# Kernel optimization log

Measured on AMD Instinct MI355X. Metric: run time of the kernel, lower is better.

## Reference

```python
import jax, jax.numpy as jnp
import numpy as np

P_EPS = 1e-6            # nn.PairwiseDistance default eps
ALPHA = 0.25
STD_TARGET = 1.0
NUM_COMMUNITIES = 512   # C = number of unique community ids
BIG = 1e30              # masking value for hard-negative min


def setup_inputs() -> dict:
    key = jax.random.key(0)
    k1, k2, k3 = jax.random.split(key, 3)
    B, N, D, C = 1, 100000, 128, NUM_COMMUNITIES
    node_features = jax.random.normal(k1, (B, N, D), dtype=jnp.float32)
    # row 0: a permutation of node indices; row 1: community of that node.
    perm = jax.random.permutation(k2, N).astype(jnp.int32)
    comm_per_node = jnp.concatenate([
        jnp.arange(C, dtype=jnp.int32),  # guarantee every community appears
        jax.random.randint(k3, (N - C,), 0, C, dtype=jnp.int32),
    ])
    community_belong_list = jnp.stack([perm, comm_per_node[perm]])  # [2, N]
    return {"node_features": node_features, "community_belong_list": community_belong_list}


def reference(node_features, community_belong_list):
    B, N, D = node_features.shape
    C = NUM_COMMUNITIES
    dt = node_features.dtype

    # ---- _community_inverse_permute: invert row-0 permutation, reorder columns ----
    perm = community_belong_list[0]
    inv = jnp.zeros((N,), perm.dtype).at[perm].add(jnp.arange(N, dtype=perm.dtype))
    cbl = community_belong_list[:, inv]          # row0 == arange(N) after this
    comm = cbl[1]                                # [N] community id per node
    src = node_features[:, cbl[0], :]            # [B,N,D] gather (identity order)

    # ---- groupby sum / count -> community means ----
    comm_sum = jnp.zeros((B, C, D), dt).at[:, comm, :].add(src)        # [B,C,D]
    counts = jnp.zeros((C,), dt).at[comm].add(jnp.asarray(1.0, dt))   # [C]
    comm_mean = comm_sum / counts[None, :, None]                      # [B,C,D]

    # ---- cdist(node_features, comm_mean, p=2) -> [B,N,C] ----
    x2 = jnp.sum(node_features * node_features, -1)                   # [B,N]
    c2 = jnp.sum(comm_mean * comm_mean, -1)                           # [B,C]
    dots = jnp.einsum('bnd,bcd->bnc', node_features, comm_mean)
    distance = jnp.sqrt(jnp.maximum(x2[:, :, None] + c2[:, None, :] - 2.0 * dots, 0.0))

    # ---- leave-one-out community mean per node, positive distance ----
    cnt_pn = counts[comm]                                             # [N]
    cnt_m1 = jnp.maximum(cnt_pn - 1.0, 1.0)                           # [N]
    x_minus = jnp.where((cnt_pn == 1.0)[None, :, None], jnp.asarray(0.0, dt), src)
    loo_mean = (comm_sum[:, comm, :] - x_minus) / cnt_m1[None, :, None]
    pos_dist = jnp.sqrt(jnp.sum((loo_mean - src + P_EPS) ** 2, -1))   # [B,N]

    # ---- negatives: all communities except the node's own ----
    own = distance[:, jnp.arange(N), comm]                            # [B,N]
    mean_neg = (jnp.sum(distance, -1) - own) / (C - 1)                # [B,N]
    pos_mask = jnp.zeros((N, C), bool).at[jnp.arange(N), comm].set(True)
    hard_neg = jnp.min(jnp.where(pos_mask[None], jnp.asarray(BIG, dt), distance), -1)

    trip_mean = jnp.maximum(pos_dist - mean_neg + ALPHA, 0.0)
    trip_min = jnp.maximum(pos_dist - hard_neg + ALPHA, 0.0)

    # ---- groupby std (unbiased) per community per feature ----
    sq = jnp.zeros((B, C, D), dt).at[:, comm, :].add((src - comm_mean[:, comm, :]) ** 2)
    std = jnp.sqrt(sq / jnp.maximum(counts - 1.0, 1.0)[None, :, None])

    return (trip_mean.mean(), trip_min.mean(), ((std - STD_TARGET) ** 2).mean())
```

## Files before the change

### kernel.cpp

```cpp
#include <hip/hip_runtime.h>

#define NCOMM 512
#define DIM   128
#define ALPHA 0.25f
#define PEPS  1e-6f
#define BIGF  1e30f
#define TILE_C 16
#define NT    (NCOMM / TILE_C)

typedef __attribute__((ext_vector_type(8))) _Float16 f16x8;
typedef __attribute__((ext_vector_type(4))) float f32x4;

#define GLOAD_LDS16(g, l) __builtin_amdgcn_global_load_lds( \
    (const __attribute__((address_space(1))) void*)(g), \
    (__attribute__((address_space(3))) void*)(l), 16, 0, 0)


__global__ void k_prep(const int* __restrict__ cbl, int* __restrict__ comm,
                       int* __restrict__ counts, int N) {
    __shared__ int h[NCOMM];
    int t = threadIdx.x;
    h[t] = 0; h[t + 256] = 0;
    __syncthreads();
    int i = blockIdx.x * 256 + t;
    if (i < N) {
        int p = cbl[i];
        int c = cbl[N + i];
        comm[p] = c;
        atomicAdd(&h[c], 1);
    }
    __syncthreads();
    int v = h[t];        if (v) atomicAdd(&counts[t], v);
    v = h[t + 256];      if (v) atomicAdd(&counts[t + 256], v);
}

__global__ void k_scan(const int* __restrict__ counts, int* __restrict__ offsets,
                       int* __restrict__ cursor, float* __restrict__ countf) {
    __shared__ int sc[NCOMM];
    int t = threadIdx.x;
    int v0 = counts[t];
    sc[t] = v0;
    __syncthreads();
    for (int off = 1; off < NCOMM; off <<= 1) {
        int v = (t >= off) ? sc[t - off] : 0;
        __syncthreads();
        sc[t] += v;
        __syncthreads();
    }
    int excl = sc[t] - v0;
    offsets[t] = excl;
    cursor[t]  = excl;
    countf[t]  = (float)v0;
}

__global__ void k_sort(const int* __restrict__ comm, int* __restrict__ cursor,
                       int* __restrict__ sorted, int N) {
    __shared__ int h[NCOMM], hb[NCOMM];
    int t = threadIdx.x;
    h[t] = 0; h[t + 256] = 0;
    __syncthreads();
    int j0 = blockIdx.x * 1024 + t;
    int cs[4];
    #pragma unroll
    for (int q = 0; q < 4; ++q) {
        int j = j0 + q * 256;
        cs[q] = (j < N) ? comm[j] : -1;
        if (cs[q] >= 0) atomicAdd(&h[cs[q]], 1);
    }
    __syncthreads();
    int v = h[t];        if (v) hb[t] = atomicAdd(&cursor[t], v);
    v = h[t + 256];      if (v) hb[t + 256] = atomicAdd(&cursor[t + 256], v);
    __syncthreads();
    #pragma unroll
    for (int q = 0; q < 4; ++q) {
        int j = j0 + q * 256;
        if (cs[q] >= 0) {
            int p = atomicAdd(&hb[cs[q]], 1);
            sorted[p] = j;
        }
    }
}


__global__ void __launch_bounds__(256) k_stats(
        const float* __restrict__ NF,
        const int* __restrict__ sorted, const int* __restrict__ offsets,
        const int* __restrict__ counts,
        float* __restrict__ comm_sum,
        _Float16* __restrict__ CMh,
        float* __restrict__ c2, float* __restrict__ accum) {
    __shared__ int ridx[512];
    __shared__ float4 bufS[256], bufQ[256];
    int c = blockIdx.x, t = threadIdx.x;
    int d4 = t & 31, r = t >> 5;
    int cnt = counts[c], base = offsets[c];
    const float4* NF4 = (const float4*)NF;

    float4 s4 = make_float4(0.f, 0.f, 0.f, 0.f);
    float4 q4 = make_float4(0.f, 0.f, 0.f, 0.f);
    for (int chunk = 0; chunk < cnt; chunk += 512) {
        int m = min(cnt - chunk, 512);
        for (int i = t; i < m; i += 256) ridx[i] = sorted[base + chunk + i];
        __syncthreads();
        int i = r;
        for (; i + 24 < m; i += 32) {
            int a0 = ridx[i], a1 = ridx[i + 8], a2 = ridx[i + 16], a3 = ridx[i + 24];
            float4 v0 = NF4[(size_t)a0 * 32 + d4];
            float4 v1 = NF4[(size_t)a1 * 32 + d4];
            float4 v2 = NF4[(size_t)a2 * 32 + d4];
            float4 v3 = NF4[(size_t)a3 * 32 + d4];
            s4.x += v0.x; s4.y += v0.y; s4.z += v0.z; s4.w += v0.w;
            q4.x = fmaf(v0.x, v0.x, q4.x); q4.y = fmaf(v0.y, v0.y, q4.y);
            q4.z = fmaf(v0.z, v0.z, q4.z); q4.w = fmaf(v0.w, v0.w, q4.w);
            s4.x += v1.x; s4.y += v1.y; s4.z += v1.z; s4.w += v1.w;
            q4.x = fmaf(v1.x, v1.x, q4.x); q4.y = fmaf(v1.y, v1.y, q4.y);
            q4.z = fmaf(v1.z, v1.z, q4.z); q4.w = fmaf(v1.w, v1.w, q4.w);
            s4.x += v2.x; s4.y += v2.y; s4.z += v2.z; s4.w += v2.w;
            q4.x = fmaf(v2.x, v2.x, q4.x); q4.y = fmaf(v2.y, v2.y, q4.y);
            q4.z = fmaf(v2.z, v2.z, q4.z); q4.w = fmaf(v2.w, v2.w, q4.w);
            s4.x += v3.x; s4.y += v3.y; s4.z += v3.z; s4.w += v3.w;
            q4.x = fmaf(v3.x, v3.x, q4.x); q4.y = fmaf(v3.y, v3.y, q4.y);
            q4.z = fmaf(v3.z, v3.z, q4.z); q4.w = fmaf(v3.w, v3.w, q4.w);
        }
        for (; i < m; i += 8) {
            float4 v = NF4[(size_t)ridx[i] * 32 + d4];
            s4.x += v.x; s4.y += v.y; s4.z += v.z; s4.w += v.w;
            q4.x = fmaf(v.x, v.x, q4.x); q4.y = fmaf(v.y, v.y, q4.y);
            q4.z = fmaf(v.z, v.z, q4.z); q4.w = fmaf(v.w, v.w, q4.w);
        }
        __syncthreads();
    }
    bufS[t] = s4; bufQ[t] = q4;
    __syncthreads();
    if (t < 128) {
        float4 a = bufS[t], b = bufS[t + 128];
        a.x += b.x; a.y += b.y; a.z += b.z; a.w += b.w; bufS[t] = a;
        float4 e = bufQ[t], f = bufQ[t + 128];
        e.x += f.x; e.y += f.y; e.z += f.z; e.w += f.w; bufQ[t] = e;
    }
    __syncthreads();
    if (t < 64) {
        float4 a = bufS[t], b = bufS[t + 64];
        a.x += b.x; a.y += b.y; a.z += b.z; a.w += b.w; bufS[t] = a;
        float4 e = bufQ[t], f = bufQ[t + 64];
        e.x += f.x; e.y += f.y; e.z += f.z; e.w += f.w; bufQ[t] = e;
    }
    __syncthreads();
    if (t < 32) {
        float4 a = bufS[t], b = bufS[t + 32];
        a.x += b.x; a.y += b.y; a.z += b.z; a.w += b.w;
        float4 e = bufQ[t], f = bufQ[t + 32];
        e.x += f.x; e.y += f.y; e.z += f.z; e.w += f.w;
        float sarr[4] = {a.x, a.y, a.z, a.w};
        float qarr[4] = {e.x, e.y, e.z, e.w};
        float cf = (float)cnt;
        float mm = 0.f, ee = 0.f;
        #pragma unroll
        for (int k = 0; k < 4; ++k) {
            int d = t * 4 + k;
            float s = sarr[k];
            comm_sum[c * DIM + d] = s;
            float m = (cnt > 0) ? s / cf : 0.f;
            CMh[c * DIM + d] = (_Float16)m;
            float varn = fmaxf(fmaf(-cf * m, m, qarr[k]), 0.f);
            float stdv = sqrtf(varn / fmaxf(cf - 1.f, 1.f));
            float er = stdv - 1.f;
            mm = fmaf(m, m, mm);
            ee = fmaf(er, er, ee);
        }
        #pragma unroll
        for (int msk = 1; msk < 32; msk <<= 1) {
            mm += __shfl_xor(mm, msk);
            ee += __shfl_xor(ee, msk);
        }
        if (t == 0) {
            c2[c] = mm;
            atomicAdd(&accum[2], ee);
        }
    }
}


__global__ void __launch_bounds__(256, 4) k_main(
        const float* __restrict__ NF,
        const _Float16* __restrict__ CMh,
        const float* __restrict__ comm_sum,
        const float* __restrict__ c2g,
        const float* __restrict__ countf,
        const int* __restrict__ comm,
        float* __restrict__ accum, int N) {
    __shared__ _Float16 Bst[4][4][TILE_C * 64];
    __shared__ float c2s[NCOMM];
    __shared__ int   comms[128];
    __shared__ float x2sh[128];
    __shared__ float sums[128], mins[128];
    __shared__ float red[8];

    int tid = threadIdx.x;
    int w  = tid >> 6;
    int l  = tid & 63;
    int lr = l & 15;
    int lk = l >> 4;
    int n0 = blockIdx.x * 128;

    int off0 = ((l >> 3) << 7) + (((l & 7) ^ ((l >> 3) & 7)) << 3);
    const _Float16* gsrc = CMh + off0;
    auto stage = [&](int ss, int b) {
        const _Float16* g = gsrc + (size_t)(ss >> 1) * 2048 + (ss & 1) * 64;
        _Float16* lh = &Bst[w][b][0];
        GLOAD_LDS16(g,        lh);
        GLOAD_LDS16(g + 1024, lh + 512);
    };
    stage(0, 0); stage(1, 1); stage(2, 2);

    c2s[tid]       = c2g[tid];
    c2s[tid + 256] = c2g[tid + 256];
    if (tid < 128) {
        int gn = n0 + tid;
        comms[tid] = (gn < N) ? comm[gn] : -1;
    }

    f16x8 ah[2][4];
    #pragma unroll
    for (int mf = 0; mf < 2; ++mf) {
        int n = n0 + w * 32 + mf * 16 + lr;
        const float4* src = (const float4*)NF + (size_t)n * 32 + lk * 2;
        float p2 = 0.f;
        #pragma unroll
        for (int ks = 0; ks < 4; ++ks) {
            float4 v0 = make_float4(0.f, 0.f, 0.f, 0.f), v1 = v0;
            if (n < N) { v0 = src[ks * 8]; v1 = src[ks * 8 + 1]; }
            float fr[8] = {v0.x, v0.y, v0.z, v0.w, v1.x, v1.y, v1.z, v1.w};
            f16x8 hh;
            #pragma unroll
            for (int t = 0; t < 8; ++t) {
                hh[t] = (_Float16)fr[t];
                p2 = fmaf(fr[t], fr[t], p2);
            }
            ah[mf][ks] = hh;
        }
        p2 += __shfl_xor(p2, 16);
        p2 += __shfl_xor(p2, 32);
        if (lk == 0) x2sh[w * 32 + mf * 16 + lr] = -0.5f * p2;
    }
    __syncthreads();

    f32x4 x2v[2];
    int cnv[2][4];
    float sumv[2][4], minv[2][4];
    #pragma unroll
    for (int mf = 0; mf < 2; ++mf) {
        x2v[mf] = *(const f32x4*)&x2sh[w * 32 + mf * 16 + lk * 4];
        #pragma unroll
        for (int j = 0; j < 4; ++j) {
            cnv[mf][j] = comms[w * 32 + mf * 16 + lk * 4 + j];
            sumv[mf][j] = 0.f; minv[mf][j] = BIGF;
        }
    }

    for (int tt = 0; tt < NT; ++tt) {
        f32x4 acc0, acc1;
        {
            int ssn = 2 * tt + 3;
            if (ssn < 64) stage(ssn, ssn & 3);
            if (tt <= 30) { asm volatile("s_waitcnt vmcnt(6)" ::: "memory"); }
            else          { asm volatile("s_waitcnt vmcnt(2)" ::: "memory"); }
            __builtin_amdgcn_sched_barrier(0);
            const _Float16* bp = &Bst[w][(2 * tt) & 3][0];
            acc0 = x2v[0]; acc1 = x2v[1];
            #pragma unroll
            for (int ks2 = 0; ks2 < 2; ++ks2) {
                int ch = (ks2 * 4 + lk) ^ (lr & 7);
                f16x8 b = *(const f16x8*)&bp[(size_t)(lr * 64 + ch * 8)];
                acc0 = __builtin_amdgcn_mfma_f32_16x16x32_f16(ah[0][ks2], b, acc0, 0, 0, 0);
                acc1 = __builtin_amdgcn_mfma_f32_16x16x32_f16(ah[1][ks2], b, acc1, 0, 0, 0);
            }
        }
        {
            int ssn = 2 * tt + 4;
            if (ssn < 64) stage(ssn, ssn & 3);
            if (tt <= 29)      { asm volatile("s_waitcnt vmcnt(6)" ::: "memory"); }
            else if (tt == 30) { asm volatile("s_waitcnt vmcnt(4)" ::: "memory"); }
            else               { asm volatile("s_waitcnt vmcnt(0)" ::: "memory"); }
            __builtin_amdgcn_sched_barrier(0);
            const _Float16* bp = &Bst[w][(2 * tt + 1) & 3][0];
            #pragma unroll
            for (int ks2 = 0; ks2 < 2; ++ks2) {
                int ch = (ks2 * 4 + lk) ^ (lr & 7);
                f16x8 b = *(const f16x8*)&bp[(size_t)(lr * 64 + ch * 8)];
                acc0 = __builtin_amdgcn_mfma_f32_16x16x32_f16(ah[0][2 + ks2], b, acc0, 0, 0, 0);
                acc1 = __builtin_amdgcn_mfma_f32_16x16x32_f16(ah[1][2 + ks2], b, acc1, 0, 0, 0);
            }
            int ccol = tt * TILE_C + lr;
            float c2v = c2s[ccol];
            #pragma unroll
            for (int j = 0; j < 4; ++j) {
                float d2a = fmaf(-2.f, acc0[j], c2v);
                float da  = __builtin_amdgcn_sqrtf(fmaxf(d2a, 0.f));
                sumv[0][j] += da;
                minv[0][j] = fminf(minv[0][j], (cnv[0][j] == ccol) ? BIGF : da);
                float d2b = fmaf(-2.f, acc1[j], c2v);
                float db  = __builtin_amdgcn_sqrtf(fmaxf(d2b, 0.f));
                sumv[1][j] += db;
                minv[1][j] = fminf(minv[1][j], (cnv[1][j] == ccol) ? BIGF : db);
            }
        }
    }

    #pragma unroll
    for (int mf = 0; mf < 2; ++mf)
        #pragma unroll
        for (int j = 0; j < 4; ++j) {
            float sv = sumv[mf][j], mv = minv[mf][j];
            #pragma unroll
            for (int msk = 1; msk < 16; msk <<= 1) {
                sv += __shfl_xor(sv, msk);
                mv = fminf(mv, __shfl_xor(mv, msk));
            }
            if (lr == 0) {
                int idx = w * 32 + mf * 16 + lk * 4 + j;
                sums[idx] = sv; mins[idx] = mv;
            }
        }
    __syncthreads();

    float tmean = 0.f, tminv = 0.f;
    {
        int ln = tid >> 1, half = tid & 1;
        int n = n0 + ln;
        if (n < N) {
            int cnode = comms[ln];
            float cf  = countf[cnode];
            float cm1 = fmaxf(cf - 1.f, 1.f);
            float rs  = 1.f / cm1;
            bool single = (cf == 1.f);
            const float4* srow = (const float4*)NF + (size_t)n * 32 + half * 16;
            const float4* csum = (const float4*)(comm_sum + (size_t)cnode * DIM) + half * 16;
            float q = 0.f, dot = 0.f;
            #pragma unroll
            for (int m = 0; m < 16; ++m) {
                float4 sv = srow[m];
                float4 cs = csum[m];
                float4 xm = single ? make_float4(0.f, 0.f, 0.f, 0.f) : sv;
                float lx = (cs.x - xm.x) * rs - sv.x + PEPS;
                float ly = (cs.y - xm.y) * rs - sv.y + PEPS;
                float lz = (cs.z - xm.z) * rs - sv.z + PEPS;
                float lw = (cs.w - xm.w) * rs - sv.w + PEPS;
                q = fmaf(lx, lx, fmaf(ly, ly, fmaf(lz, lz, fmaf(lw, lw, q))));
                dot = fmaf(sv.x, cs.x, fmaf(sv.y, cs.y, fmaf(sv.z, cs.z, fmaf(sv.w, cs.w, dot))));
            }
            q   += __shfl_xor(q, 1);
            dot += __shfl_xor(dot, 1);
            if (half == 0) {
                float pos = sqrtf(q);
                float x2 = -2.f * x2sh[ln];
                float ownd2 = x2 + c2s[cnode] - 2.f * (dot / cf);
                float own = sqrtf(fmaxf(ownd2, 0.f));
                float mean_neg = (sums[ln] - own) * (1.f / (float)(NCOMM - 1));
                tmean = fmaxf(pos - mean_neg + ALPHA, 0.f);
                tminv = fmaxf(pos - mins[ln] + ALPHA, 0.f);
            }
        }
    }
    #pragma unroll
    for (int msk = 1; msk < 64; msk <<= 1) {
        tmean += __shfl_xor(tmean, msk);
        tminv += __shfl_xor(tminv, msk);
    }
    if ((tid & 63) == 0) { red[w * 2] = tmean; red[w * 2 + 1] = tminv; }
    __syncthreads();
    if (tid == 0) {
        atomicAdd(&accum[0], red[0] + red[2] + red[4] + red[6]);
        atomicAdd(&accum[1], red[1] + red[3] + red[5] + red[7]);
    }
}

__global__ void k_final(const float* __restrict__ accum, float* __restrict__ out, int N) {
    if (threadIdx.x == 0) {
        out[0] = accum[0] / (float)N;
        out[1] = accum[1] / (float)N;
        out[2] = accum[2] / (float)(NCOMM * DIM);
    }
}


extern "C" void kernel_launch(void* const* d_in, const int* in_sizes, int n_in,
                              void* d_out, int out_size, void* d_ws, size_t ws_size,
                              hipStream_t stream) {
    const float* NF  = (const float*)d_in[0];
    const int*   CBL = (const int*)d_in[1];
    int N = in_sizes[1] / 2;
    if (N <= 0) return;

    char* ws = (char*)d_ws;
    float* accum   = (float*)ws;
    int*   counts  = (int*)(ws + 16);
    int*   cursor  = (int*)(ws + 16 + 2048);
    int*   offsets = (int*)(ws + 16 + 2 * 2048);
    float* countf  = (float*)(ws + 16 + 3 * 2048);
    float* c2      = (float*)(ws + 16 + 4 * 2048);
    char* p = ws + 16 + 5 * 2048;
    int* comm   = (int*)p; p += (size_t)N * 4;
    int* sorted = (int*)p; p += (size_t)N * 4;
    float* comm_sum = (float*)p; p += (size_t)NCOMM * DIM * 4;
    _Float16* CMh = (_Float16*)p;

    hipMemsetAsync(d_ws, 0, 16 + 2048, stream);

    int nb = (N + 255) / 256;
    k_prep<<<nb, 256, 0, stream>>>(CBL, comm, counts, N);
    k_scan<<<1, NCOMM, 0, stream>>>(counts, offsets, cursor, countf);
    int nb4 = (N + 1023) / 1024;
    k_sort<<<nb4, 256, 0, stream>>>(comm, cursor, sorted, N);
    k_stats<<<NCOMM, 256, 0, stream>>>(NF, sorted, offsets, counts,
                                       comm_sum, CMh, c2, accum);
    int mb = (N + 127) / 128;
    k_main<<<mb, 256, 0, stream>>>(NF, CMh, comm_sum, c2, countf,
                                   comm, accum, N);
    k_final<<<1, 64, 0, stream>>>(accum, (float*)d_out, N);
}
```

Before: 119.6 us.

## Fold scan and final kernels into last-block epilogues, unroll stats gather, raise MFMA priority

Removes the separate k_scan and k_final launches. The last block to finish k_prep now does the 512-entry prefix scan, and the last block of k_main writes the outputs, both detected with an atomic done counter. The gather loop in k_stats is unrolled from 4 to 8 loads per iteration to keep more memory requests in flight, and s_setprio wraps the MFMA sections in k_main. The aim is less launch overhead and better latency hiding, at the cost of extra atomics, threadfences and more register pressure.

```diff
diff --git a/kernel.cpp b/kernel.cpp
--- a/kernel.cpp
+++ b/kernel.cpp
@@ -17,8 +17,12 @@
 
 
 __global__ void k_prep(const int* __restrict__ cbl, int* __restrict__ comm,
-                       int* __restrict__ counts, int N) {
+                       int* __restrict__ counts, int* __restrict__ done,
+                       int* __restrict__ cursor, int* __restrict__ offsets,
+                       float* __restrict__ countf, int N) {
     __shared__ int h[NCOMM];
+    __shared__ int sc[NCOMM];
+    __shared__ int lastFlag;
     int t = threadIdx.x;
     h[t] = 0; h[t + 256] = 0;
     __syncthreads();
@@ -32,25 +36,30 @@
     __syncthreads();
     int v = h[t];        if (v) atomicAdd(&counts[t], v);
     v = h[t + 256];      if (v) atomicAdd(&counts[t + 256], v);
-}
-
-__global__ void k_scan(const int* __restrict__ counts, int* __restrict__ offsets,
-                       int* __restrict__ cursor, float* __restrict__ countf) {
-    __shared__ int sc[NCOMM];
-    int t = threadIdx.x;
-    int v0 = counts[t];
-    sc[t] = v0;
+
+    __threadfence();
+    __syncthreads();
+    if (t == 0) lastFlag = (atomicAdd(done, 1) == (int)gridDim.x - 1) ? 1 : 0;
+    __syncthreads();
+    if (!lastFlag) return;
+
+    int a0 = atomicAdd(&counts[t], 0);
+    int a1 = atomicAdd(&counts[t + 256], 0);
+    sc[t] = a0; sc[t + 256] = a1;
     __syncthreads();
     for (int off = 1; off < NCOMM; off <<= 1) {
-        int v = (t >= off) ? sc[t - off] : 0;
+        int x0 = (t >= off) ? sc[t - off] : 0;
+        int x1 = (t + 256 >= off) ? sc[t + 256 - off] : 0;
         __syncthreads();
-        sc[t] += v;
+        sc[t] += x0; sc[t + 256] += x1;
         __syncthreads();
     }
-    int excl = sc[t] - v0;
-    offsets[t] = excl;
-    cursor[t]  = excl;
-    countf[t]  = (float)v0;
+    offsets[t]       = sc[t] - a0;
+    cursor[t]        = sc[t] - a0;
+    countf[t]        = (float)a0;
+    offsets[t + 256] = sc[t + 256] - a1;
+    cursor[t + 256]  = sc[t + 256] - a1;
+    countf[t + 256]  = (float)a1;
 }
 
 __global__ void k_sort(const int* __restrict__ comm, int* __restrict__ cursor,
@@ -103,12 +112,17 @@
         for (int i = t; i < m; i += 256) ridx[i] = sorted[base + chunk + i];
         __syncthreads();
         int i = r;
-        for (; i + 24 < m; i += 32) {
-            int a0 = ridx[i], a1 = ridx[i + 8], a2 = ridx[i + 16], a3 = ridx[i + 24];
+        for (; i + 56 < m; i += 64) {
+            int a0 = ridx[i],      a1 = ridx[i + 8],  a2 = ridx[i + 16], a3 = ridx[i + 24];
+            int a4 = ridx[i + 32], a5 = ridx[i + 40], a6 = ridx[i + 48], a7 = ridx[i + 56];
             float4 v0 = NF4[(size_t)a0 * 32 + d4];
             float4 v1 = NF4[(size_t)a1 * 32 + d4];
             float4 v2 = NF4[(size_t)a2 * 32 + d4];
             float4 v3 = NF4[(size_t)a3 * 32 + d4];
+            float4 v4 = NF4[(size_t)a4 * 32 + d4];
+            float4 v5 = NF4[(size_t)a5 * 32 + d4];
+            float4 v6 = NF4[(size_t)a6 * 32 + d4];
+            float4 v7 = NF4[(size_t)a7 * 32 + d4];
             s4.x += v0.x; s4.y += v0.y; s4.z += v0.z; s4.w += v0.w;
             q4.x = fmaf(v0.x, v0.x, q4.x); q4.y = fmaf(v0.y, v0.y, q4.y);
             q4.z = fmaf(v0.z, v0.z, q4.z); q4.w = fmaf(v0.w, v0.w, q4.w);
@@ -121,6 +135,18 @@
             s4.x += v3.x; s4.y += v3.y; s4.z += v3.z; s4.w += v3.w;
             q4.x = fmaf(v3.x, v3.x, q4.x); q4.y = fmaf(v3.y, v3.y, q4.y);
             q4.z = fmaf(v3.z, v3.z, q4.z); q4.w = fmaf(v3.w, v3.w, q4.w);
+            s4.x += v4.x; s4.y += v4.y; s4.z += v4.z; s4.w += v4.w;
+            q4.x = fmaf(v4.x, v4.x, q4.x); q4.y = fmaf(v4.y, v4.y, q4.y);
+            q4.z = fmaf(v4.z, v4.z, q4.z); q4.w = fmaf(v4.w, v4.w, q4.w);
+            s4.x += v5.x; s4.y += v5.y; s4.z += v5.z; s4.w += v5.w;
+            q4.x = fmaf(v5.x, v5.x, q4.x); q4.y = fmaf(v5.y, v5.y, q4.y);
+            q4.z = fmaf(v5.z, v5.z, q4.z); q4.w = fmaf(v5.w, v5.w, q4.w);
+            s4.x += v6.x; s4.y += v6.y; s4.z += v6.z; s4.w += v6.w;
+            q4.x = fmaf(v6.x, v6.x, q4.x); q4.y = fmaf(v6.y, v6.y, q4.y);
+            q4.z = fmaf(v6.z, v6.z, q4.z); q4.w = fmaf(v6.w, v6.w, q4.w);
+            s4.x += v7.x; s4.y += v7.y; s4.z += v7.z; s4.w += v7.w;
+            q4.x = fmaf(v7.x, v7.x, q4.x); q4.y = fmaf(v7.y, v7.y, q4.y);
+            q4.z = fmaf(v7.z, v7.z, q4.z); q4.w = fmaf(v7.w, v7.w, q4.w);
         }
         for (; i < m; i += 8) {
             float4 v = NF4[(size_t)ridx[i] * 32 + d4];
@@ -188,7 +214,8 @@
         const float* __restrict__ c2g,
         const float* __restrict__ countf,
         const int* __restrict__ comm,
-        float* __restrict__ accum, int N) {
+        float* __restrict__ accum, int* __restrict__ done,
+        float* __restrict__ out, int N) {
     __shared__ _Float16 Bst[4][4][TILE_C * 64];
     __shared__ float c2s[NCOMM];
     __shared__ int   comms[128];
@@ -268,6 +295,7 @@
             __builtin_amdgcn_sched_barrier(0);
             const _Float16* bp = &Bst[w][(2 * tt) & 3][0];
             acc0 = x2v[0]; acc1 = x2v[1];
+            __builtin_amdgcn_s_setprio(1);
             #pragma unroll
             for (int ks2 = 0; ks2 < 2; ++ks2) {
                 int ch = (ks2 * 4 + lk) ^ (lr & 7);
@@ -275,6 +303,7 @@
                 acc0 = __builtin_amdgcn_mfma_f32_16x16x32_f16(ah[0][ks2], b, acc0, 0, 0, 0);
                 acc1 = __builtin_amdgcn_mfma_f32_16x16x32_f16(ah[1][ks2], b, acc1, 0, 0, 0);
             }
+            __builtin_amdgcn_s_setprio(0);
         }
         {
             int ssn = 2 * tt + 4;
@@ -284,6 +313,7 @@
             else               { asm volatile("s_waitcnt vmcnt(0)" ::: "memory"); }
             __builtin_amdgcn_sched_barrier(0);
             const _Float16* bp = &Bst[w][(2 * tt + 1) & 3][0];
+            __builtin_amdgcn_s_setprio(1);
             #pragma unroll
             for (int ks2 = 0; ks2 < 2; ++ks2) {
                 int ch = (ks2 * 4 + lk) ^ (lr & 7);
@@ -291,6 +321,7 @@
                 acc0 = __builtin_amdgcn_mfma_f32_16x16x32_f16(ah[0][2 + ks2], b, acc0, 0, 0, 0);
                 acc1 = __builtin_amdgcn_mfma_f32_16x16x32_f16(ah[1][2 + ks2], b, acc1, 0, 0, 0);
             }
+            __builtin_amdgcn_s_setprio(0);
             int ccol = tt * TILE_C + lr;
             float c2v = c2s[ccol];
             #pragma unroll
@@ -372,14 +403,15 @@
     if (tid == 0) {
         atomicAdd(&accum[0], red[0] + red[2] + red[4] + red[6]);
         atomicAdd(&accum[1], red[1] + red[3] + red[5] + red[7]);
-    }
-}
-
-__global__ void k_final(const float* __restrict__ accum, float* __restrict__ out, int N) {
-    if (threadIdx.x == 0) {
-        out[0] = accum[0] / (float)N;
-        out[1] = accum[1] / (float)N;
-        out[2] = accum[2] / (float)(NCOMM * DIM);
+        __threadfence();
+        if (atomicAdd(done, 1) == (int)gridDim.x - 1) {
+            float a0 = atomicAdd(&accum[0], 0.f);
+            float a1 = atomicAdd(&accum[1], 0.f);
+            float a2 = atomicAdd(&accum[2], 0.f);
+            out[0] = a0 / (float)N;
+            out[1] = a1 / (float)N;
+            out[2] = a2 / (float)(NCOMM * DIM);
+        }
     }
 }
 
@@ -394,28 +426,27 @@
 
     char* ws = (char*)d_ws;
     float* accum   = (float*)ws;
-    int*   counts  = (int*)(ws + 16);
-    int*   cursor  = (int*)(ws + 16 + 2048);
-    int*   offsets = (int*)(ws + 16 + 2 * 2048);
-    float* countf  = (float*)(ws + 16 + 3 * 2048);
-    float* c2      = (float*)(ws + 16 + 4 * 2048);
-    char* p = ws + 16 + 5 * 2048;
+    int*   done    = (int*)(ws + 16);
+    int*   counts  = (int*)(ws + 32);
+    int*   cursor  = (int*)(ws + 32 + 2048);
+    int*   offsets = (int*)(ws + 32 + 2 * 2048);
+    float* countf  = (float*)(ws + 32 + 3 * 2048);
+    float* c2      = (float*)(ws + 32 + 4 * 2048);
+    char* p = ws + 32 + 5 * 2048;
     int* comm   = (int*)p; p += (size_t)N * 4;
     int* sorted = (int*)p; p += (size_t)N * 4;
     float* comm_sum = (float*)p; p += (size_t)NCOMM * DIM * 4;
     _Float16* CMh = (_Float16*)p;
 
-    hipMemsetAsync(d_ws, 0, 16 + 2048, stream);
+    hipMemsetAsync(d_ws, 0, 32 + 2048, stream);
 
     int nb = (N + 255) / 256;
-    k_prep<<<nb, 256, 0, stream>>>(CBL, comm, counts, N);
-    k_scan<<<1, NCOMM, 0, stream>>>(counts, offsets, cursor, countf);
+    k_prep<<<nb, 256, 0, stream>>>(CBL, comm, counts, done, cursor, offsets, countf, N);
     int nb4 = (N + 1023) / 1024;
     k_sort<<<nb4, 256, 0, stream>>>(comm, cursor, sorted, N);
     k_stats<<<NCOMM, 256, 0, stream>>>(NF, sorted, offsets, counts,
                                        comm_sum, CMh, c2, accum);
     int mb = (N + 127) / 128;
     k_main<<<mb, 256, 0, stream>>>(NF, CMh, comm_sum, c2, countf,
-                                   comm, accum, N);
-    k_final<<<1, 64, 0, stream>>>(accum, (float*)d_out, N);
+                                   comm, accum, done + 1, (float*)d_out, N);
 }
```

Measured after the change: 159.0 us. 1.33x slower.
